# Optimization experiments

Measured on AMD Instinct MI355X. Metric: run time of the kernel, lower is better.

The kernel has to match this reference:

```python
import jax, jax.numpy as jnp
import numpy as np

NHEAD = 8
ATTN_EPS = 1e-6
LN_EPS = 1e-5


def _layernorm(y, g, b):
    mu = jnp.mean(y, axis=-1, keepdims=True)
    var = jnp.var(y, axis=-1, keepdims=True)
    return (y - mu) * jax.lax.rsqrt(var + LN_EPS) * g + b


def setup_inputs() -> dict:
    key = jax.random.key(0)
    ks = jax.random.split(key, 6)
    B, L, D = 2, 8192, 1024
    s = 1.0 / np.sqrt(D)
    return {
        "x": jax.random.normal(ks[0], (B, L, D), jnp.float32),
        "Wq": jax.random.normal(ks[1], (D, D), jnp.float32) * s,
        "Wm": jax.random.normal(ks[2], (D, D), jnp.float32) * s,
        "W1": jax.random.normal(ks[3], (D, 2 * D), jnp.float32) * s,
        "W2": jax.random.normal(ks[4], (2 * D, D), jnp.float32) * (1.0 / np.sqrt(2 * D)),
        "g1": jnp.ones((D,), jnp.float32),
        "b1": jnp.zeros((D,), jnp.float32),
        "g2": jnp.ones((D,), jnp.float32),
        "b2": jnp.zeros((D,), jnp.float32),
    }


def reference(x, Wq, Wm, W1, W2, g1, b1, g2, b2):
    B, L, D = x.shape
    H = NHEAD
    d = D // H
    # NOTE: original forward uses q_proj for query, key AND value (faithful).
    q = (x @ Wq).reshape(B, L, H, d)  # [B,L,H,d]
    feat = jax.nn.elu(q) + 1.0        # elu feature map, shared by Q and K
    Q = feat
    K = feat
    V = q / L                          # value = value / v_length
    # KV outer-product sum over sequence: [B,H,d,d]
    KV = jnp.einsum('nshd,nshv->nhdv', K, V)
    # normalizer Z: [B,L,H]
    Ksum = K.sum(axis=1)               # [B,H,d]
    Z = 1.0 / (jnp.einsum('nlhd,nhd->nlh', Q, Ksum) + ATTN_EPS)
    msg = jnp.einsum('nlhd,nhdv,nlh->nlhv', Q, KV, Z) * L  # [B,L,H,d]
    msg = msg.reshape(B, L, D) @ Wm    # merge heads
    x = x + _layernorm(msg, g1, b1)
    # NOTE: MLP is applied to `message`, not the updated x (faithful to source).
    mlp = jax.nn.relu(msg @ W1) @ W2
    x = x + _layernorm(mlp, g2, b2)
    return x
```

## Files before the change

### kernel.cpp

```cpp
#include <hip/hip_runtime.h>
#include <hip/hip_bf16.h>
#include <stdint.h>

#define AS1 __attribute__((address_space(1)))
#define AS3 __attribute__((address_space(3)))

typedef __bf16 bf16x8 __attribute__((ext_vector_type(8)));
typedef float  f32x4  __attribute__((ext_vector_type(4)));

static constexpr int kL   = 8192;
static constexpr int kD   = 1024;
static constexpr int kM   = 2 * kL;
static constexpr int kNCH = 32;
static constexpr int kSCH = kL / kNCH;

__device__ __forceinline__ void async_cp16(__bf16* lds, const __bf16* g) {
    __builtin_amdgcn_global_load_lds((AS1 uint32_t*)g, (AS3 uint32_t*)lds, 16, 0, 0);
}

__device__ __forceinline__ float elu1f(float x) {
    return x > 0.0f ? x + 1.0f : __expf(x);
}

template <int M0>
__device__ __forceinline__ void mfma16(f32x4 (&acc)[8][4], const bf16x8 (&af)[4],
                                       const bf16x8 (&bq)[4]) {
#pragma unroll
    for (int i = 0; i < 4; ++i)
#pragma unroll
        for (int n = 0; n < 4; ++n)
            acc[M0 + i][n] = __builtin_amdgcn_mfma_f32_16x16x32_bf16(af[i], bq[n], acc[M0 + i][n], 0, 0, 0);
}

template <int EPI>
__global__ __launch_bounds__(512, 2) void gemm256(const __bf16* __restrict__ A,
                                                  const __bf16* __restrict__ Bt,
                                                  __bf16* __restrict__ C,
                                                  int M, int N, int K) {
    __shared__ __bf16 As[32768];
    __shared__ __bf16 Bs[32768];
    const int tid  = threadIdx.x;
    const int w    = tid >> 6;
    const int l    = tid & 63;
    const int quad = l >> 4;
    const int l16  = l & 15;
    const int wm   = w >> 2;
    const int wn   = w & 3;
    const int row0 = blockIdx.x * 256;
    const int col0 = blockIdx.y * 256;

    const int srow = l >> 2;
    const int sc   = ((l & 3) - (srow >> 1)) & 3;
    const __bf16* Ag0 = A  + (size_t)(row0 + w * 32 + srow) * K + sc * 8;
    const __bf16* Bg0 = Bt + (size_t)(col0 + w * 32 + srow) * K + sc * 8;
    const size_t r16K = (size_t)16 * K;
    const int NT = K >> 6;

    const int fpos = ((quad + (l16 >> 1)) & 3) * 8;
    const int arow = wm * 4096 + l16 * 32 + fpos;
    const int brow = wn * 2048 + l16 * 32 + fpos;

    f32x4 acc[8][4] = {};

    auto stage_h = [&](int ts, int hh) {
        if (ts >= NT) return;
        const int off = (ts & 1) * 16384 + (hh >> 1) * 8192 + w * 1024;
        const int ko  = ts * 64 + (hh >> 1) * 32;
        if ((hh & 1) == 0) {
            async_cp16(&As[off], Ag0 + ko);
            async_cp16(&As[off + 512], Ag0 + ko + r16K);
        } else {
            async_cp16(&Bs[off], Bg0 + ko);
            async_cp16(&Bs[off + 512], Bg0 + ko + r16K);
        }
    };

    stage_h(0, 0); stage_h(0, 1); stage_h(0, 2); stage_h(0, 3);
    asm volatile("s_waitcnt vmcnt(4)" ::: "memory");
    stage_h(1, 0); stage_h(1, 1); stage_h(1, 2);
    asm volatile("s_waitcnt vmcnt(6)" ::: "memory");
    __builtin_amdgcn_s_barrier();

    for (int t = 0; t < NT; ++t) {
        const int bo = (t & 1) * 16384;
        bf16x8 af[4], bq[4];

#pragma unroll
        for (int i = 0; i < 4; ++i) af[i] = *(const bf16x8*)&As[bo + arow + i * 512];
#pragma unroll
        for (int n = 0; n < 4; ++n) bq[n] = *(const bf16x8*)&Bs[bo + brow + n * 512];
        stage_h(t + 1, 3);
        __builtin_amdgcn_s_barrier();
        asm volatile("s_waitcnt lgkmcnt(0)" ::: "memory");
        __builtin_amdgcn_sched_barrier(0);
        __builtin_amdgcn_s_setprio(1);
        mfma16<0>(acc, af, bq);
        __builtin_amdgcn_s_setprio(0);
        __builtin_amdgcn_s_barrier();

#pragma unroll
        for (int i = 0; i < 4; ++i) af[i] = *(const bf16x8*)&As[bo + arow + 2048 + i * 512];
        stage_h(t + 2, 0);
        __builtin_amdgcn_s_barrier();
        asm volatile("s_waitcnt lgkmcnt(0)" ::: "memory");
        __builtin_amdgcn_sched_barrier(0);
        __builtin_amdgcn_s_setprio(1);
        mfma16<4>(acc, af, bq);
        __builtin_amdgcn_s_setprio(0);
        __builtin_amdgcn_s_barrier();

#pragma unroll
        for (int i = 0; i < 4; ++i) af[i] = *(const bf16x8*)&As[bo + 8192 + arow + i * 512];
#pragma unroll
        for (int n = 0; n < 4; ++n) bq[n] = *(const bf16x8*)&Bs[bo + 8192 + brow + n * 512];
        stage_h(t + 2, 1);
        __builtin_amdgcn_s_barrier();
        asm volatile("s_waitcnt lgkmcnt(0)" ::: "memory");
        __builtin_amdgcn_sched_barrier(0);
        __builtin_amdgcn_s_setprio(1);
        mfma16<0>(acc, af, bq);
        __builtin_amdgcn_s_setprio(0);
        __builtin_amdgcn_s_barrier();

#pragma unroll
        for (int i = 0; i < 4; ++i) af[i] = *(const bf16x8*)&As[bo + 8192 + arow + 2048 + i * 512];
        stage_h(t + 2, 2);
        __builtin_amdgcn_s_barrier();
        asm volatile("s_waitcnt lgkmcnt(0)" ::: "memory");
        __builtin_amdgcn_sched_barrier(0);
        __builtin_amdgcn_s_setprio(1);
        mfma16<4>(acc, af, bq);
        __builtin_amdgcn_s_setprio(0);
        if (t + 2 < NT)       { asm volatile("s_waitcnt vmcnt(6)" ::: "memory"); }
        else if (t + 2 == NT) { asm volatile("s_waitcnt vmcnt(0)" ::: "memory"); }
        __builtin_amdgcn_s_barrier();
    }

#pragma unroll
    for (int m = 0; m < 8; ++m) {
        const int rowb = row0 + wm * 128 + m * 16 + quad * 4;
#pragma unroll
        for (int n = 0; n < 4; ++n) {
            const int col = col0 + wn * 64 + n * 16 + l16;
#pragma unroll
            for (int r = 0; r < 4; ++r) {
                float v = acc[m][n][r];
                if (EPI == 1) v = v > 0.0f ? v : 0.0f;
                C[(size_t)(rowb + r) * N + col] = (__bf16)v;
            }
        }
    }
    (void)M;
}

__global__ __launch_bounds__(256) void cvt_f2b(const float* __restrict__ in,
                                               __bf16* __restrict__ out) {
    const size_t i = ((size_t)blockIdx.x * 256 + threadIdx.x) * 8;
    f32x4 a = *(const f32x4*)(in + i);
    f32x4 b = *(const f32x4*)(in + i + 4);
    bf16x8 o;
#pragma unroll
    for (int j = 0; j < 4; ++j) { o[j] = (__bf16)a[j]; o[4 + j] = (__bf16)b[j]; }
    *(bf16x8*)(out + i) = o;
}

__global__ __launch_bounds__(256) void transpose_f2b(const float* __restrict__ in,
                                                     __bf16* __restrict__ out,
                                                     int R, int Ccols) {
    __shared__ __bf16 tile[32][33];
    const int bc = blockIdx.x * 32;
    const int br = blockIdx.y * 32;
    const int tx = threadIdx.x & 31;
    const int ty = threadIdx.x >> 5;
#pragma unroll
    for (int i = ty; i < 32; i += 8)
        tile[i][tx] = (__bf16)in[(size_t)(br + i) * Ccols + bc + tx];
    __syncthreads();
#pragma unroll
    for (int i = ty; i < 32; i += 8)
        out[(size_t)(bc + i) * R + br + tx] = tile[tx][i];
}

__global__ __launch_bounds__(256) void kv_partial(const __bf16* __restrict__ q,
                                                  float* __restrict__ KVpart,
                                                  float* __restrict__ Kspart) {
    __shared__ __bf16 fs[64 * 128];
    __shared__ __bf16 qs[64 * 128];
    const int bh = blockIdx.x;
    const int ch = blockIdx.y;
    const int b = bh >> 3, h = bh & 7;
    const int t = threadIdx.x;
    const int dk0 = (t >> 4) * 8;
    const int dv0 = (t & 15) * 8;
    const int s0 = ch * kSCH;
    const size_t rowbase = ((size_t)b * kL) * kD + (size_t)h * 128;

    float acc[8][8] = {};
    float ksacc[8] = {};

    for (int st = 0; st < kSCH / 64; ++st) {
        if (st) __syncthreads();
#pragma unroll
        for (int c = 0; c < 4; ++c) {
            int id = c * 256 + t;
            int r = id >> 4;
            int col = (id & 15) * 8;
            bf16x8 qv = *(const bf16x8*)(q + rowbase + (size_t)(s0 + st * 64 + r) * kD + col);
            *(bf16x8*)&qs[r * 128 + col] = qv;
            bf16x8 fv;
#pragma unroll
            for (int j = 0; j < 8; ++j) fv[j] = (__bf16)elu1f((float)qv[j]);
            *(bf16x8*)&fs[r * 128 + col] = fv;
        }
        __syncthreads();
        for (int s = 0; s < 64; ++s) {
            bf16x8 fv = *(const bf16x8*)&fs[s * 128 + dk0];
            bf16x8 qv = *(const bf16x8*)&qs[s * 128 + dv0];
            float fk[8], vv[8];
#pragma unroll
            for (int i = 0; i < 8; ++i) { fk[i] = (float)fv[i]; vv[i] = (float)qv[i]; }
#pragma unroll
            for (int i = 0; i < 8; ++i)
#pragma unroll
                for (int j = 0; j < 8; ++j)
                    acc[i][j] += fk[i] * vv[j];
#pragma unroll
            for (int i = 0; i < 8; ++i) ksacc[i] += fk[i];
        }
    }

    float* outp = KVpart + (((size_t)bh * kNCH + ch) << 14) + (size_t)dk0 * 128 + dv0;
#pragma unroll
    for (int i = 0; i < 8; ++i) {
        f32x4 w0, w1;
#pragma unroll
        for (int j = 0; j < 4; ++j) { w0[j] = acc[i][j]; w1[j] = acc[i][j + 4]; }
        *(f32x4*)(outp + i * 128) = w0;
        *(f32x4*)(outp + i * 128 + 4) = w1;
    }
    if ((t & 15) == 0) {
        float* kp = Kspart + ((size_t)bh * kNCH + ch) * 128 + dk0;
#pragma unroll
        for (int i = 0; i < 8; ++i) kp[i] = ksacc[i];
    }
}

__global__ __launch_bounds__(256) void reduce_kv(const float* __restrict__ KVpart,
                                                 const float* __restrict__ Kspart,
                                                 __bf16* __restrict__ KVb,
                                                 float* __restrict__ Ksum) {
    const int t = threadIdx.x;
    if (blockIdx.x < 1024) {
        const size_t o = (size_t)blockIdx.x * 256 + t;
        const size_t bh = o >> 14;
        const size_t rem = o & 16383;
        float s = 0.f;
#pragma unroll 4
        for (int ch = 0; ch < kNCH; ++ch)
            s += KVpart[((bh * kNCH + ch) << 14) + rem];
        KVb[o] = (__bf16)s;
    } else {
        const int o = (blockIdx.x - 1024) * 256 + t;
        const int bh = o >> 7;
        const int dk = o & 127;
        float s = 0.f;
#pragma unroll 4
        for (int ch = 0; ch < kNCH; ++ch)
            s += Kspart[(bh * kNCH + ch) * 128 + dk];
        Ksum[o] = s;
    }
}

__global__ __launch_bounds__(256) void msg_kernel(const __bf16* __restrict__ q,
                                                  const __bf16* __restrict__ KVb,
                                                  const float* __restrict__ Ks,
                                                  __bf16* __restrict__ msg) {
    __shared__ __bf16 fls[64 * 128];
    __shared__ __bf16 kvs[128 * 128];
    __shared__ float KsS[128];
    const int bh = blockIdx.x, b = bh >> 3, h = bh & 7;
    const int rbase = blockIdx.y * 64;
    const int t = threadIdx.x;
    const size_t rowbase = ((size_t)b * kL) * kD + (size_t)h * 128;

#pragma unroll
    for (int c = 0; c < 4; ++c) {
        int id = c * 256 + t;
        int r = id >> 4, col = (id & 15) * 8;
        bf16x8 qv = *(const bf16x8*)(q + rowbase + (size_t)(rbase + r) * kD + col);
        bf16x8 fv;
#pragma unroll
        for (int j = 0; j < 8; ++j) fv[j] = (__bf16)elu1f((float)qv[j]);
        *(bf16x8*)&fls[r * 128 + col] = fv;
    }
    {
        const __bf16* kvg = KVb + ((size_t)bh << 14);
#pragma unroll
        for (int c = 0; c < 8; ++c) {
            int id = c * 256 + t;
            *(bf16x8*)&kvs[id * 8] = *(const bf16x8*)(kvg + id * 8);
        }
    }
    if (t < 32) *(f32x4*)&KsS[t * 4] = *(const f32x4*)(Ks + bh * 128 + t * 4);
    __syncthreads();

    const int rg = t >> 4, c = t & 15, dv0 = c * 8;
    float Zi[4];
#pragma unroll
    for (int i = 0; i < 4; ++i) {
        int r = rg + i * 16;
        float p = 0.f;
#pragma unroll
        for (int j = 0; j < 8; ++j)
            p += (float)fls[r * 128 + c * 8 + j] * KsS[c * 8 + j];
        p += __shfl_xor(p, 1, 16);
        p += __shfl_xor(p, 2, 16);
        p += __shfl_xor(p, 4, 16);
        p += __shfl_xor(p, 8, 16);
        Zi[i] = 1.0f / (p + 1e-6f);
    }

    float acc[4][8] = {};
#pragma unroll 2
    for (int dk = 0; dk < 128; ++dk) {
        bf16x8 kvv = *(const bf16x8*)&kvs[dk * 128 + dv0];
        float kf[8];
#pragma unroll
        for (int j = 0; j < 8; ++j) kf[j] = (float)kvv[j];
        float fv[4];
#pragma unroll
        for (int i = 0; i < 4; ++i) fv[i] = (float)fls[(rg + i * 16) * 128 + dk];
#pragma unroll
        for (int i = 0; i < 4; ++i)
#pragma unroll
            for (int j = 0; j < 8; ++j)
                acc[i][j] += fv[i] * kf[j];
    }

#pragma unroll
    for (int i = 0; i < 4; ++i) {
        bf16x8 o;
#pragma unroll
        for (int j = 0; j < 8; ++j) o[j] = (__bf16)(acc[i][j] * Zi[i]);
        *(bf16x8*)(msg + rowbase + (size_t)(rbase + rg + i * 16) * kD + dv0) = o;
    }
}

template <int BF16BASE>
__global__ __launch_bounds__(256) void ln_res(const void* __restrict__ basep,
                                              const __bf16* __restrict__ y,
                                              const float* __restrict__ g,
                                              const float* __restrict__ bvec,
                                              float* __restrict__ out) {
    const int wave = threadIdx.x >> 6, lane = threadIdx.x & 63;
    const int row = blockIdx.x * 4 + wave;
    const size_t ro = (size_t)row * kD + lane * 16;
    bf16x8 y0 = *(const bf16x8*)(y + ro);
    bf16x8 y1 = *(const bf16x8*)(y + ro + 8);
    float v[16];
    float s = 0.f, sq = 0.f;
#pragma unroll
    for (int j = 0; j < 8; ++j) { v[j] = (float)y0[j]; v[8 + j] = (float)y1[j]; }
#pragma unroll
    for (int j = 0; j < 16; ++j) { s += v[j]; sq += v[j] * v[j]; }
#pragma unroll
    for (int m = 1; m < 64; m <<= 1) { s += __shfl_xor(s, m); sq += __shfl_xor(sq, m); }
    const float mu = s * (1.0f / 1024.0f);
    float var = sq * (1.0f / 1024.0f) - mu * mu;
    if (var < 0.f) var = 0.f;
    const float rstd = rsqrtf(var + 1e-5f);
    const int go = lane * 16;
    float bs[16];
    if (BF16BASE) {
        bf16x8 b0 = *(const bf16x8*)((const __bf16*)basep + ro);
        bf16x8 b1 = *(const bf16x8*)((const __bf16*)basep + ro + 8);
#pragma unroll
        for (int j = 0; j < 8; ++j) { bs[j] = (float)b0[j]; bs[8 + j] = (float)b1[j]; }
    } else {
#pragma unroll
        for (int j = 0; j < 4; ++j) {
            f32x4 bb = *(const f32x4*)((const float*)basep + ro + j * 4);
#pragma unroll
            for (int r = 0; r < 4; ++r) bs[j * 4 + r] = bb[r];
        }
    }
#pragma unroll
    for (int j = 0; j < 4; ++j) {
        f32x4 gg = *(const f32x4*)(g + go + j * 4);
        f32x4 be = *(const f32x4*)(bvec + go + j * 4);
        f32x4 o;
#pragma unroll
        for (int r = 0; r < 4; ++r)
            o[r] = bs[j * 4 + r] + (v[j * 4 + r] - mu) * rstd * gg[r] + be[r];
        *(f32x4*)(out + ro + j * 4) = o;
    }
}

extern "C" void kernel_launch(void* const* d_in, const int* in_sizes, int n_in,
                              void* d_out, int out_size, void* d_ws, size_t ws_size,
                              hipStream_t stream) {
    const float* x  = (const float*)d_in[0];
    const float* Wq = (const float*)d_in[1];
    const float* Wm = (const float*)d_in[2];
    const float* W1 = (const float*)d_in[3];
    const float* W2 = (const float*)d_in[4];
    const float* g1 = (const float*)d_in[5];
    const float* b1 = (const float*)d_in[6];
    const float* g2 = (const float*)d_in[7];
    const float* b2 = (const float*)d_in[8];
    float* out = (float*)d_out;

    const size_t BLD = (size_t)kM * kD;
    __bf16* q    = (__bf16*)d_ws;
    __bf16* msg  = q + BLD;
    __bf16* hbuf = msg + BLD;
    __bf16* WqT  = hbuf + 2 * BLD;
    __bf16* WmT  = WqT + 1048576;
    __bf16* W1T  = WmT + 1048576;
    __bf16* W2T  = W1T + 2097152;
    __bf16* KVb  = W2T + 2097152;
    float* KVpart = (float*)(KVb + 262144);
    float* Kspart = KVpart + (size_t)kNCH * 16 * 16384;
    float* Ksum   = Kspart + (size_t)16 * kNCH * 128;
    const size_t need = ((char*)(Ksum + 2048)) - (char*)d_ws;
    if (ws_size < need) return;

    __bf16* xb   = hbuf;
    __bf16* msg2 = q;
    __bf16* mlp  = msg;

    const dim3 blk(256);
    const dim3 blk5(512);

    cvt_f2b<<<dim3((unsigned)(BLD / 2048)), blk, 0, stream>>>(x, xb);
    transpose_f2b<<<dim3(32, 32), blk, 0, stream>>>(Wq, WqT, kD, kD);
    transpose_f2b<<<dim3(32, 32), blk, 0, stream>>>(Wm, WmT, kD, kD);
    transpose_f2b<<<dim3(64, 32), blk, 0, stream>>>(W1, W1T, kD, 2048);
    transpose_f2b<<<dim3(32, 64), blk, 0, stream>>>(W2, W2T, 2048, kD);

    gemm256<0><<<dim3(kM / 256, kD / 256), blk5, 0, stream>>>(xb, WqT, q, kM, kD, kD);
    kv_partial<<<dim3(16, kNCH), blk, 0, stream>>>(q, KVpart, Kspart);
    reduce_kv<<<dim3(1032), blk, 0, stream>>>(KVpart, Kspart, KVb, Ksum);
    msg_kernel<<<dim3(16, kL / 64), blk, 0, stream>>>(q, KVb, Ksum, msg);
    gemm256<0><<<dim3(kM / 256, kD / 256), blk5, 0, stream>>>(msg, WmT, msg2, kM, kD, kD);
    ln_res<1><<<dim3(kM / 4), blk, 0, stream>>>(xb, msg2, g1, b1, out);
    gemm256<1><<<dim3(kM / 256, 2048 / 256), blk5, 0, stream>>>(msg2, W1T, hbuf, kM, 2048, kD);
    gemm256<0><<<dim3(kM / 256, kD / 256), blk5, 0, stream>>>(hbuf, W2T, mlp, kM, kD, 2048);
    ln_res<0><<<dim3(kM / 4), blk, 0, stream>>>(out, mlp, g2, b2, out);
    (void)in_sizes; (void)n_in; (void)out_size;
}
```

Baseline: 549.1 us.

## Move KV and message attention contractions onto MFMA with transposed feature layouts

Replaces the scalar FMA kv_partial and msg_kernel with MFMA-based GEMM kernels that use double-buffered async global-to-LDS loads. A new transpose_q kernel writes sequence-major transposed copies of q and the ELU feature, and overwrites q in place with the feature. The normalizer Z moves into a separate z_kernel, and reduce_kv now writes KV transposed so it can feed the MFMA B operand. The aim is to cut the FP32 ALU cost of the two attention contractions, in exchange for an extra transpose pass over q, more launches, and scalar (uncoalesced) element stores in the epilogues.

```diff
diff --git a/kernel.cpp b/kernel.cpp
--- a/kernel.cpp
+++ b/kernel.cpp
@@ -6,13 +6,13 @@
 #define AS3 __attribute__((address_space(3)))
 
 typedef __bf16 bf16x8 __attribute__((ext_vector_type(8)));
+typedef __bf16 bf16x2 __attribute__((ext_vector_type(2)));
 typedef float  f32x4  __attribute__((ext_vector_type(4)));
 
 static constexpr int kL   = 8192;
 static constexpr int kD   = 1024;
 static constexpr int kM   = 2 * kL;
 static constexpr int kNCH = 32;
-static constexpr int kSCH = kL / kNCH;
 
 __device__ __forceinline__ void async_cp16(__bf16* lds, const __bf16* g) {
     __builtin_amdgcn_global_load_lds((AS1 uint32_t*)g, (AS3 uint32_t*)lds, 16, 0, 0);
@@ -181,73 +181,143 @@
         out[(size_t)(bc + i) * R + br + tx] = tile[tx][i];
 }
 
-__global__ __launch_bounds__(256) void kv_partial(const __bf16* __restrict__ q,
-                                                  float* __restrict__ KVpart,
-                                                  float* __restrict__ Kspart) {
-    __shared__ __bf16 fs[64 * 128];
-    __shared__ __bf16 qs[64 * 128];
-    const int bh = blockIdx.x;
-    const int ch = blockIdx.y;
-    const int b = bh >> 3, h = bh & 7;
+__global__ __launch_bounds__(256) void transpose_q(__bf16* __restrict__ q_io,
+                                                   __bf16* __restrict__ qT,
+                                                   __bf16* __restrict__ fT) {
+    __shared__ __bf16 qs[64 * 130];
+    __shared__ __bf16 fs[64 * 130];
+    const int bh = blockIdx.x, b = bh >> 3, h = bh & 7;
+    const int s0 = blockIdx.y * 64;
     const int t = threadIdx.x;
-    const int dk0 = (t >> 4) * 8;
-    const int dv0 = (t & 15) * 8;
-    const int s0 = ch * kSCH;
-    const size_t rowbase = ((size_t)b * kL) * kD + (size_t)h * 128;
-
-    float acc[8][8] = {};
-    float ksacc[8] = {};
-
-    for (int st = 0; st < kSCH / 64; ++st) {
-        if (st) __syncthreads();
-#pragma unroll
-        for (int c = 0; c < 4; ++c) {
-            int id = c * 256 + t;
-            int r = id >> 4;
-            int col = (id & 15) * 8;
-            bf16x8 qv = *(const bf16x8*)(q + rowbase + (size_t)(s0 + st * 64 + r) * kD + col);
-            *(bf16x8*)&qs[r * 128 + col] = qv;
-            bf16x8 fv;
-#pragma unroll
-            for (int j = 0; j < 8; ++j) fv[j] = (__bf16)elu1f((float)qv[j]);
-            *(bf16x8*)&fs[r * 128 + col] = fv;
-        }
+    const size_t rowbase = (size_t)b * 8388608 + (size_t)h * 128;
+
+#pragma unroll
+    for (int c = 0; c < 4; ++c) {
+        const int id = c * 256 + t;
+        const int r = id >> 4, col = (id & 15) * 8;
+        __bf16* gp = q_io + rowbase + (size_t)(s0 + r) * 1024 + col;
+        bf16x8 qv = *(const bf16x8*)gp;
+        bf16x8 fv;
+#pragma unroll
+        for (int j = 0; j < 8; ++j) fv[j] = (__bf16)elu1f((float)qv[j]);
+        *(bf16x8*)gp = fv;
+        const int lb = r * 130 + col;
+#pragma unroll
+        for (int p = 0; p < 4; ++p) {
+            bf16x2 qp = { qv[2 * p], qv[2 * p + 1] };
+            bf16x2 fp_ = { fv[2 * p], fv[2 * p + 1] };
+            *(bf16x2*)&qs[lb + 2 * p] = qp;
+            *(bf16x2*)&fs[lb + 2 * p] = fp_;
+        }
+    }
+    __syncthreads();
+
+    const size_t ob = (size_t)bh * (128 * 8192) + s0;
+#pragma unroll
+    for (int c = 0; c < 4; ++c) {
+        const int id = c * 256 + t;
+        const int dk = id >> 3, sch = id & 7;
+        bf16x8 ov, fo;
+#pragma unroll
+        for (int j = 0; j < 8; ++j) {
+            ov[j] = qs[(sch * 8 + j) * 130 + dk];
+            fo[j] = fs[(sch * 8 + j) * 130 + dk];
+        }
+        *(bf16x8*)(qT + ob + (size_t)dk * 8192 + sch * 8) = ov;
+        *(bf16x8*)(fT + ob + (size_t)dk * 8192 + sch * 8) = fo;
+    }
+}
+
+__global__ __launch_bounds__(256) void kv_gemm(const __bf16* __restrict__ fT,
+                                               const __bf16* __restrict__ qT,
+                                               float* __restrict__ KVpart,
+                                               float* __restrict__ Kspart) {
+    __shared__ __bf16 As[2][128 * 32];
+    __shared__ __bf16 Bs[2][128 * 32];
+    const int tid  = threadIdx.x;
+    const int wave = tid >> 6, lane = tid & 63;
+    const int quad = lane >> 4, l16 = lane & 15;
+    const int wm = wave & 1, wn = wave >> 1;
+    const int bh = blockIdx.x, ch = blockIdx.y;
+
+    f32x4 acc[4][4] = {};
+    float ksacc[4] = {};
+
+    const int srow = lane >> 2;
+    const int sk8  = ((lane & 3) - (srow >> 1)) & 3;
+    const size_t base = (size_t)bh * (128 * 8192) + ch * 256 + sk8 * 8;
+    const __bf16* Ag0 = fT + base + (size_t)(wave * 32 + srow) * 8192;
+    const __bf16* Bg0 = qT + base + (size_t)(wave * 32 + srow) * 8192;
+    const size_t r16 = (size_t)16 * 8192;
+    const int ldsw = wave * 1024;
+    const int fp = ((quad + (l16 >> 1)) & 3) * 8;
+    const int frow = l16 * 32 + fp;
+    const int nk = 8;
+    {
+        async_cp16(&As[0][ldsw], Ag0);
+        async_cp16(&As[0][ldsw + 512], Ag0 + r16);
+        async_cp16(&Bs[0][ldsw], Bg0);
+        async_cp16(&Bs[0][ldsw + 512], Bg0 + r16);
+    }
+    for (int k = 0; k < nk; ++k) {
         __syncthreads();
-        for (int s = 0; s < 64; ++s) {
-            bf16x8 fv = *(const bf16x8*)&fs[s * 128 + dk0];
-            bf16x8 qv = *(const bf16x8*)&qs[s * 128 + dv0];
-            float fk[8], vv[8];
-#pragma unroll
-            for (int i = 0; i < 8; ++i) { fk[i] = (float)fv[i]; vv[i] = (float)qv[i]; }
-#pragma unroll
-            for (int i = 0; i < 8; ++i)
-#pragma unroll
-                for (int j = 0; j < 8; ++j)
-                    acc[i][j] += fk[i] * vv[j];
-#pragma unroll
-            for (int i = 0; i < 8; ++i) ksacc[i] += fk[i];
-        }
-    }
-
-    float* outp = KVpart + (((size_t)bh * kNCH + ch) << 14) + (size_t)dk0 * 128 + dv0;
-#pragma unroll
-    for (int i = 0; i < 8; ++i) {
-        f32x4 w0, w1;
-#pragma unroll
-        for (int j = 0; j < 4; ++j) { w0[j] = acc[i][j]; w1[j] = acc[i][j + 4]; }
-        *(f32x4*)(outp + i * 128) = w0;
-        *(f32x4*)(outp + i * 128 + 4) = w1;
-    }
-    if ((t & 15) == 0) {
-        float* kp = Kspart + ((size_t)bh * kNCH + ch) * 128 + dk0;
-#pragma unroll
-        for (int i = 0; i < 8; ++i) kp[i] = ksacc[i];
+        if (k + 1 < nk) {
+            const int nb = (k + 1) & 1;
+            const int ko = (k + 1) << 5;
+            async_cp16(&As[nb][ldsw], Ag0 + ko);
+            async_cp16(&As[nb][ldsw + 512], Ag0 + r16 + ko);
+            async_cp16(&Bs[nb][ldsw], Bg0 + ko);
+            async_cp16(&Bs[nb][ldsw + 512], Bg0 + r16 + ko);
+        }
+        const __bf16* Asb = As[k & 1];
+        const __bf16* Bsb = Bs[k & 1];
+        bf16x8 af[4], bfr[4];
+#pragma unroll
+        for (int i = 0; i < 4; ++i)
+            af[i] = *(const bf16x8*)&Asb[(wm * 4 + i) * 512 + frow];
+#pragma unroll
+        for (int j = 0; j < 4; ++j)
+            bfr[j] = *(const bf16x8*)&Bsb[(wn * 4 + j) * 512 + frow];
+        if (wn == 0) {
+#pragma unroll
+            for (int i = 0; i < 4; ++i)
+#pragma unroll
+                for (int j = 0; j < 8; ++j) ksacc[i] += (float)af[i][j];
+        }
+#pragma unroll
+        for (int i = 0; i < 4; ++i)
+#pragma unroll
+            for (int j = 0; j < 4; ++j)
+                acc[i][j] = __builtin_amdgcn_mfma_f32_16x16x32_bf16(af[i], bfr[j], acc[i][j], 0, 0, 0);
+    }
+
+    float* outp = KVpart + (((size_t)bh * kNCH + ch) << 14);
+#pragma unroll
+    for (int i = 0; i < 4; ++i) {
+        const int rowb = wm * 64 + i * 16 + quad * 4;
+#pragma unroll
+        for (int j = 0; j < 4; ++j) {
+            const int col = wn * 64 + j * 16 + l16;
+#pragma unroll
+            for (int r = 0; r < 4; ++r)
+                outp[(rowb + r) * 128 + col] = acc[i][j][r];
+        }
+    }
+    if (wn == 0) {
+#pragma unroll
+        for (int i = 0; i < 4; ++i) {
+            float v = ksacc[i];
+            v += __shfl_xor(v, 16);
+            v += __shfl_xor(v, 32);
+            if (quad == 0)
+                Kspart[((size_t)bh * kNCH + ch) * 128 + wm * 64 + i * 16 + l16] = v;
+        }
     }
 }
 
 __global__ __launch_bounds__(256) void reduce_kv(const float* __restrict__ KVpart,
                                                  const float* __restrict__ Kspart,
-                                                 __bf16* __restrict__ KVb,
+                                                 __bf16* __restrict__ KVbT,
                                                  float* __restrict__ Ksum) {
     const int t = threadIdx.x;
     if (blockIdx.x < 1024) {
@@ -258,7 +328,8 @@
 #pragma unroll 4
         for (int ch = 0; ch < kNCH; ++ch)
             s += KVpart[((bh * kNCH + ch) << 14) + rem];
-        KVb[o] = (__bf16)s;
+        const int dk = (int)(rem >> 7), dv = (int)(rem & 127);
+        KVbT[(bh << 14) + dv * 128 + dk] = (__bf16)s;
     } else {
         const int o = (blockIdx.x - 1024) * 256 + t;
         const int bh = o >> 7;
@@ -271,78 +342,101 @@
     }
 }
 
-__global__ __launch_bounds__(256) void msg_kernel(const __bf16* __restrict__ q,
-                                                  const __bf16* __restrict__ KVb,
-                                                  const float* __restrict__ Ks,
-                                                  __bf16* __restrict__ msg) {
-    __shared__ __bf16 fls[64 * 128];
-    __shared__ __bf16 kvs[128 * 128];
-    __shared__ float KsS[128];
+__global__ __launch_bounds__(256) void z_kernel(const __bf16* __restrict__ featG,
+                                                const float* __restrict__ Ksum,
+                                                float* __restrict__ Zbuf) {
+    __shared__ float Ks[128];
+    const int t = threadIdx.x;
+    const int id0 = blockIdx.x * 256;
+    const int bh = id0 >> 13;
+    if (t < 32) *(f32x4*)&Ks[t * 4] = *(const f32x4*)(Ksum + bh * 128 + t * 4);
+    __syncthreads();
+    const int s = (id0 + t) & 8191;
+    const int b = bh >> 3, h = bh & 7;
+    const __bf16* row = featG + (size_t)b * 8388608 + (size_t)s * 1024 + h * 128;
+    float p = 0.f;
+#pragma unroll
+    for (int c = 0; c < 16; ++c) {
+        bf16x8 v = *(const bf16x8*)(row + c * 8);
+#pragma unroll
+        for (int j = 0; j < 8; ++j) p += (float)v[j] * Ks[c * 8 + j];
+    }
+    Zbuf[(size_t)bh * 8192 + s] = 1.0f / (p + 1e-6f);
+}
+
+__global__ __launch_bounds__(256) void msg_gemm(const __bf16* __restrict__ featG,
+                                                const __bf16* __restrict__ KVbT,
+                                                const float* __restrict__ Zbuf,
+                                                __bf16* __restrict__ msg) {
+    __shared__ __bf16 As[2][128 * 32];
+    __shared__ __bf16 Bs[2][128 * 32];
+    __shared__ float Zs[128];
+    const int tid  = threadIdx.x;
+    const int wave = tid >> 6, lane = tid & 63;
+    const int quad = lane >> 4, l16 = lane & 15;
+    const int wm = wave & 1, wn = wave >> 1;
     const int bh = blockIdx.x, b = bh >> 3, h = bh & 7;
-    const int rbase = blockIdx.y * 64;
-    const int t = threadIdx.x;
-    const size_t rowbase = ((size_t)b * kL) * kD + (size_t)h * 128;
-
-#pragma unroll
-    for (int c = 0; c < 4; ++c) {
-        int id = c * 256 + t;
-        int r = id >> 4, col = (id & 15) * 8;
-        bf16x8 qv = *(const bf16x8*)(q + rowbase + (size_t)(rbase + r) * kD + col);
-        bf16x8 fv;
-#pragma unroll
-        for (int j = 0; j < 8; ++j) fv[j] = (__bf16)elu1f((float)qv[j]);
-        *(bf16x8*)&fls[r * 128 + col] = fv;
-    }
+    const int row0 = blockIdx.y * 128;
+
+    if (tid < 32)
+        *(f32x4*)&Zs[tid * 4] = *(const f32x4*)(Zbuf + (size_t)bh * 8192 + row0 + tid * 4);
+
+    f32x4 acc[4][4] = {};
+    const int srow = lane >> 2;
+    const int sk8  = ((lane & 3) - (srow >> 1)) & 3;
+    const __bf16* Ag0 = featG + (size_t)b * 8388608 + (size_t)(row0 + wave * 32 + srow) * 1024 + h * 128 + sk8 * 8;
+    const __bf16* Bg0 = KVbT + ((size_t)bh << 14) + (wave * 32 + srow) * 128 + sk8 * 8;
+    const size_t rA16 = (size_t)16 * 1024;
+    const size_t rB16 = (size_t)16 * 128;
+    const int ldsw = wave * 1024;
+    const int fp = ((quad + (l16 >> 1)) & 3) * 8;
+    const int frow = l16 * 32 + fp;
+    const int nk = 4;
     {
-        const __bf16* kvg = KVb + ((size_t)bh << 14);
-#pragma unroll
-        for (int c = 0; c < 8; ++c) {
-            int id = c * 256 + t;
-            *(bf16x8*)&kvs[id * 8] = *(const bf16x8*)(kvg + id * 8);
-        }
-    }
-    if (t < 32) *(f32x4*)&KsS[t * 4] = *(const f32x4*)(Ks + bh * 128 + t * 4);
-    __syncthreads();
-
-    const int rg = t >> 4, c = t & 15, dv0 = c * 8;
-    float Zi[4];
+        async_cp16(&As[0][ldsw], Ag0);
+        async_cp16(&As[0][ldsw + 512], Ag0 + rA16);
+        async_cp16(&Bs[0][ldsw], Bg0);
+        async_cp16(&Bs[0][ldsw + 512], Bg0 + rB16);
+    }
+    for (int k = 0; k < nk; ++k) {
+        __syncthreads();
+        if (k + 1 < nk) {
+            const int nb = (k + 1) & 1;
+            const int ko = (k + 1) << 5;
+            async_cp16(&As[nb][ldsw], Ag0 + ko);
+            async_cp16(&As[nb][ldsw + 512], Ag0 + rA16 + ko);
+            async_cp16(&Bs[nb][ldsw], Bg0 + ko);
+            async_cp16(&Bs[nb][ldsw + 512], Bg0 + rB16 + ko);
+        }
+        const __bf16* Asb = As[k & 1];
+        const __bf16* Bsb = Bs[k & 1];
+        bf16x8 af[4], bfr[4];
+#pragma unroll
+        for (int i = 0; i < 4; ++i)
+            af[i] = *(const bf16x8*)&Asb[(wm * 4 + i) * 512 + frow];
+#pragma unroll
+        for (int j = 0; j < 4; ++j)
+            bfr[j] = *(const bf16x8*)&Bsb[(wn * 4 + j) * 512 + frow];
+#pragma unroll
+        for (int i = 0; i < 4; ++i)
+#pragma unroll
+            for (int j = 0; j < 4; ++j)
+                acc[i][j] = __builtin_amdgcn_mfma_f32_16x16x32_bf16(af[i], bfr[j], acc[i][j], 0, 0, 0);
+    }
+
+    const size_t obase = (size_t)b * 8388608 + (size_t)h * 128;
 #pragma unroll
     for (int i = 0; i < 4; ++i) {
-        int r = rg + i * 16;
-        float p = 0.f;
-#pragma unroll
-        for (int j = 0; j < 8; ++j)
-            p += (float)fls[r * 128 + c * 8 + j] * KsS[c * 8 + j];
-        p += __shfl_xor(p, 1, 16);
-        p += __shfl_xor(p, 2, 16);
-        p += __shfl_xor(p, 4, 16);
-        p += __shfl_xor(p, 8, 16);
-        Zi[i] = 1.0f / (p + 1e-6f);
-    }
-
-    float acc[4][8] = {};
-#pragma unroll 2
-    for (int dk = 0; dk < 128; ++dk) {
-        bf16x8 kvv = *(const bf16x8*)&kvs[dk * 128 + dv0];
-        float kf[8];
-#pragma unroll
-        for (int j = 0; j < 8; ++j) kf[j] = (float)kvv[j];
-        float fv[4];
-#pragma unroll
-        for (int i = 0; i < 4; ++i) fv[i] = (float)fls[(rg + i * 16) * 128 + dk];
-#pragma unroll
-        for (int i = 0; i < 4; ++i)
-#pragma unroll
-            for (int j = 0; j < 8; ++j)
-                acc[i][j] += fv[i] * kf[j];
-    }
-
-#pragma unroll
-    for (int i = 0; i < 4; ++i) {
-        bf16x8 o;
-#pragma unroll
-        for (int j = 0; j < 8; ++j) o[j] = (__bf16)(acc[i][j] * Zi[i]);
-        *(bf16x8*)(msg + rowbase + (size_t)(rbase + rg + i * 16) * kD + dv0) = o;
+        const int lr0 = wm * 64 + i * 16 + quad * 4;
+#pragma unroll
+        for (int j = 0; j < 4; ++j) {
+            const int col = wn * 64 + j * 16 + l16;
+#pragma unroll
+            for (int r = 0; r < 4; ++r) {
+                const float v = acc[i][j][r] * Zs[lr0 + r];
+                msg[obase + (size_t)(row0 + lr0 + r) * 1024 + col] = (__bf16)v;
+            }
+        }
     }
 }
 
@@ -426,8 +520,11 @@
     if (ws_size < need) return;
 
     __bf16* xb   = hbuf;
+    __bf16* qT   = hbuf + BLD;
+    __bf16* fT   = msg;
     __bf16* msg2 = q;
     __bf16* mlp  = msg;
+    float*  Zbuf = KVpart;
 
     const dim3 blk(256);
     const dim3 blk5(512);
@@ -439,9 +536,11 @@
     transpose_f2b<<<dim3(32, 64), blk, 0, stream>>>(W2, W2T, 2048, kD);
 
     gemm256<0><<<dim3(kM / 256, kD / 256), blk5, 0, stream>>>(xb, WqT, q, kM, kD, kD);
-    kv_partial<<<dim3(16, kNCH), blk, 0, stream>>>(q, KVpart, Kspart);
+    transpose_q<<<dim3(16, 128), blk, 0, stream>>>(q, qT, fT);
+    kv_gemm<<<dim3(16, kNCH), blk, 0, stream>>>(fT, qT, KVpart, Kspart);
     reduce_kv<<<dim3(1032), blk, 0, stream>>>(KVpart, Kspart, KVb, Ksum);
-    msg_kernel<<<dim3(16, kL / 64), blk, 0, stream>>>(q, KVb, Ksum, msg);
+    z_kernel<<<dim3(512), blk, 0, stream>>>(q, Ksum, Zbuf);
+    msg_gemm<<<dim3(16, kL / 128), blk, 0, stream>>>(q, KVb, Zbuf, msg);
     gemm256<0><<<dim3(kM / 256, kD / 256), blk5, 0, stream>>>(msg, WmT, msg2, kM, kD, kD);
     ln_res<1><<<dim3(kM / 4), blk, 0, stream>>>(xb, msg2, g1, b1, out);
     gemm256<1><<<dim3(kM / 256, 2048 / 256), blk5, 0, stream>>>(msg2, W1T, hbuf, kM, 2048, kD);
```

New measurement: 477.6 us. 13.0% less time.
